# Kernel optimization log

Measured on AMD Instinct MI355X. Metric: run time of the kernel, lower is better.

## Reference

```python
import jax, jax.numpy as jnp
import numpy as np

N_A, N_B = 50000, 20000   # authors, teams
E0, E1, E2 = 600000, 300000, 300000  # coauthor(A->A), writes(A->B), influences(B->A)
D = 128                   # in_feats = out_feats


def setup_inputs() -> dict:
    key = jax.random.key(0)
    ks = jax.random.split(key, 12)
    h_A = jax.random.normal(ks[0], (N_A, D), jnp.float32)
    h_B = jax.random.normal(ks[1], (N_B, D), jnp.float32)
    W0 = jax.random.normal(ks[2], (D, D), jnp.float32) * 0.05
    W1 = jax.random.normal(ks[3], (D, D), jnp.float32) * 0.05
    W2 = jax.random.normal(ks[4], (D, D), jnp.float32) * 0.05
    b0 = jnp.zeros((D,), jnp.float32)
    b1 = jnp.zeros((D,), jnp.float32)
    b2 = jnp.zeros((D,), jnp.float32)
    src0 = jax.random.randint(ks[5], (E0,), 0, N_A)
    dst0 = jax.random.randint(ks[6], (E0,), 0, N_A)
    src1 = jax.random.randint(ks[7], (E1,), 0, N_A)
    dst1 = jax.random.randint(ks[8], (E1,), 0, N_B)
    src2 = jax.random.randint(ks[9], (E2,), 0, N_B)
    dst2 = jax.random.randint(ks[10], (E2,), 0, N_A)
    return dict(h_A=h_A, h_B=h_B, W0=W0, b0=b0, W1=W1, b1=b1, W2=W2, b2=b2,
                src0=src0, dst0=dst0, src1=src1, dst1=dst1, src2=src2, dst2=dst2)


def _graph_conv(x_src, W, b, src, dst, n_dst):
    """DGL GraphConv, norm='both': out = D_dst^{-1/2} A D_src^{-1/2} (X W) + b."""
    n_src = x_src.shape[0]
    ones = jnp.ones(src.shape[0], x_src.dtype)
    deg_out = jnp.clip(jax.ops.segment_sum(ones, src, num_segments=n_src), 1.0)
    deg_in = jnp.clip(jax.ops.segment_sum(ones, dst, num_segments=n_dst), 1.0)
    m = (x_src @ W) * (deg_out ** -0.5)[:, None]          # [n_src, D]
    agg = jax.ops.segment_sum(m[src], dst, num_segments=n_dst)  # [n_dst, D]
    return agg * (deg_in ** -0.5)[:, None] + b


def reference(h_A, h_B, W0, b0, W1, b1, W2, b2, src0, dst0, src1, dst1, src2, dst2):
    # HeteroGraphConv(aggregate='sum'): sum per-relation GraphConv outputs per dst ntype.
    out_A = (_graph_conv(h_A, W0, b0, src0, dst0, N_A)
             + _graph_conv(h_B, W2, b2, src2, dst2, N_A))
    out_B = _graph_conv(h_A, W1, b1, src1, dst1, N_B)
    # every ntype present in h receives an output, so no passthrough branch fires
    return out_A, out_B
```

## Files before the change

kernel.cpp:

```cpp
#include <hip/hip_runtime.h>

#define NA 50000
#define NB 20000
#define NE0 600000
#define NE1 300000
#define NE2 300000
#define DD 128
#define DEG_TOT (4 * NA + 2 * NB)
#define SUB 16384
#define PER 18750

#define P_TOT 5440000

typedef short bf16x8 __attribute__((ext_vector_type(8)));
typedef float f32x4 __attribute__((ext_vector_type(4)));

__device__ __forceinline__ unsigned short f2bf(float f) {
    union { float f; unsigned int u; } v; v.f = f;
    unsigned int r = v.u + 0x7fffu + ((v.u >> 16) & 1u);
    return (unsigned short)(r >> 16);
}
__device__ __forceinline__ float bf2f(unsigned int u16) {
    union { float f; unsigned int u; } v; v.u = u16 << 16;
    return v.f;
}

__global__ __launch_bounds__(512) void hist_kernel(
    const int* __restrict__ s0, const int* __restrict__ d0,
    const int* __restrict__ s1, const int* __restrict__ d1,
    const int* __restrict__ s2, const int* __restrict__ d2,
    int* __restrict__ P,
    int* __restrict__ rank0, int* __restrict__ rank1, int* __restrict__ rank2)
{
    __shared__ int h[SUB];
    const int cfg = blockIdx.z;
    const int En[6] = {NE0, NE0, NE1, NE1, NE2, NE2};
    const int Kn[6] = {NA, NA, NA, NB, NB, NA};
    const int Gn[6] = {32, 32, 16, 16, 16, 16};
    const int Po[6] = {0, 1600000, 3200000, 4000000, 4320000, 4640000};
    int E = En[cfg], K = Kn[cfg], G = Gn[cfg];
    int sub = blockIdx.x, g = blockIdx.y;
    int nsub = (K + SUB - 1) / SUB;
    if (sub >= nsub || g >= G) return;
    const int* keys = cfg == 0 ? s0 : cfg == 1 ? d0 : cfg == 2 ? s1
                    : cfg == 3 ? d1 : cfg == 4 ? s2 : d2;
    int* rk = cfg == 1 ? rank0 : cfg == 3 ? rank1 : cfg == 5 ? rank2 : (int*)0;
    int lo = sub * SUB;
    int hi = min(K, lo + SUB);
    int cnt = hi - lo;
    for (int i = threadIdx.x; i < cnt; i += 512) h[i] = 0;
    __syncthreads();
    int e1 = min(E, g * PER + PER);
    for (int e = g * PER + threadIdx.x; e < e1; e += 512) {
        int k = keys[e];
        if (k >= lo && k < hi) {
            int r = atomicAdd(&h[k - lo], 1);
            if (rk) rk[e] = r;
        }
    }
    __syncthreads();
    int* outp = P + Po[cfg] + g * K + lo;
    for (int i = threadIdx.x; i < cnt; i += 512) outp[i] = h[i];
}

__global__ __launch_bounds__(256) void reduce_kernel(
    const int* __restrict__ P, int* __restrict__ ideg, float* __restrict__ rdeg)
{
    int i = blockIdx.x * 256 + threadIdx.x;
    if (i >= DEG_TOT) return;
    int h, k;
    if      (i < NA)            { h = 0; k = i; }
    else if (i < 2 * NA)        { h = 1; k = i - NA; }
    else if (i < 3 * NA)        { h = 2; k = i - 2 * NA; }
    else if (i < 3 * NA + NB)   { h = 3; k = i - 3 * NA; }
    else if (i < 3 * NA + 2*NB) { h = 4; k = i - 3 * NA - NB; }
    else                        { h = 5; k = i - 3 * NA - 2 * NB; }
    const int Po[6] = {0, 1600000, 3200000, 4000000, 4320000, 4640000};
    const int Gn[6] = {32, 32, 16, 16, 16, 16};
    const int Kn[6] = {NA, NA, NA, NB, NB, NA};
    const int* p = P + Po[h] + k;
    int K = Kn[h], G = Gn[h], s = 0;
    for (int g = 0; g < G; ++g) s += p[g * K];
    ideg[i] = s;
    rdeg[i] = rsqrtf(fmaxf((float)s, 1.f));
}

__global__ __launch_bounds__(256) void scan_reduce(
    const int* __restrict__ ideg, int* __restrict__ spart)
{
    __shared__ int lds[256];
    int y = blockIdx.y;
    const int off[3] = {NA, 3 * NA, 3 * NA + 2 * NB};
    const int nn[3]  = {NA, NB, NA};
    int n = nn[y];
    int b = blockIdx.x, t = threadIdx.x;
    if (b * 1024 >= n) return;
    const int* deg = ideg + off[y];
    int base = b * 1024 + t * 4;
    int s = 0;
    #pragma unroll
    for (int k = 0; k < 4; ++k) { int i = base + k; if (i < n) s += deg[i]; }
    lds[t] = s; __syncthreads();
    for (int o = 128; o > 0; o >>= 1) {
        if (t < o) lds[t] += lds[t + o];
        __syncthreads();
    }
    if (t == 0) spart[y * 64 + b] = lds[0];
}

__global__ void spine_kernel(int* __restrict__ spart) {
    int w = threadIdx.x >> 6, lane = threadIdx.x & 63;
    const int nblk[3] = {49, 20, 49};
    int n = nblk[w];
    int* p = spart + w * 64;
    int orig = (lane < n) ? p[lane] : 0;
    int v = orig;
    #pragma unroll
    for (int o = 1; o < 64; o <<= 1) {
        int u = __shfl_up(v, o);
        if (lane >= o) v += u;
    }
    if (lane < n) p[lane] = v - orig;
}

__global__ __launch_bounds__(256) void scan_final(
    const int* __restrict__ ideg, const int* __restrict__ spart,
    int* __restrict__ rp)
{
    __shared__ int lds[256];
    int y = blockIdx.y;
    const int off[3] = {NA, 3 * NA, 3 * NA + 2 * NB};
    const int nn[3]  = {NA, NB, NA};
    const int ro[3]  = {0, NA, NA + NB};
    int n = nn[y];
    int b = blockIdx.x, t = threadIdx.x;
    if (b * 1024 >= n) return;
    const int* deg = ideg + off[y];
    int* rowptr = rp + ro[y];
    int base = b * 1024 + t * 4;
    int v[4]; int tsum = 0;
    #pragma unroll
    for (int k = 0; k < 4; ++k) {
        v[k] = (base + k < n) ? deg[base + k] : 0;
        tsum += v[k];
    }
    lds[t] = tsum; __syncthreads();
    for (int o = 1; o < 256; o <<= 1) {
        int x = (t >= o) ? lds[t - o] : 0;
        __syncthreads();
        lds[t] += x;
        __syncthreads();
    }
    int run = lds[t] - tsum + spart[y * 64 + b];
    #pragma unroll
    for (int k = 0; k < 4; ++k) {
        if (base + k < n) rowptr[base + k] = run;
        run += v[k];
    }
}

__global__ __launch_bounds__(256) void offsets_kernel(
    int* __restrict__ P, const int* __restrict__ rp)
{
    int i = blockIdx.x * 256 + threadIdx.x;
    if (i >= 2 * NA + NB) return;
    int base, G, K, d, run;
    if (i < NA)           { base = 1600000; G = 32; K = NA; d = i;           run = rp[d]; }
    else if (i < NA + NB) { base = 4000000; G = 16; K = NB; d = i - NA;      run = rp[NA + d]; }
    else                  { base = 4640000; G = 16; K = NA; d = i - NA - NB; run = rp[NA + NB + d]; }
    int* p = P + base + d;
    for (int g = 0; g < G; ++g) {
        int t = p[g * K];
        p[g * K] = run;
        run += t;
    }
}

__global__ __launch_bounds__(512) void place_parallel(
    const int* __restrict__ s0, const int* __restrict__ d0,
    const int* __restrict__ s1, const int* __restrict__ d1,
    const int* __restrict__ s2, const int* __restrict__ d2,
    const int* __restrict__ P,
    const int* __restrict__ rank0, const int* __restrict__ rank1,
    const int* __restrict__ rank2,
    int* __restrict__ csr0, int* __restrict__ csr1, int* __restrict__ csr2)
{
    int z = blockIdx.z;
    const int En[3] = {NE0, NE1, NE2};
    const int Kn[3] = {NA, NB, NA};
    const int Po[3] = {1600000, 4000000, 4640000};
    int E = En[z], K = Kn[z];
    const int* src = z == 0 ? s0 : z == 1 ? s1 : s2;
    const int* dst = z == 0 ? d0 : z == 1 ? d1 : d2;
    const int* rk  = z == 0 ? rank0 : z == 1 ? rank1 : rank2;
    int* csr = z == 0 ? csr0 : z == 1 ? csr1 : csr2;
    const int* off = P + Po[z];
    int e = blockIdx.x * 512 + threadIdx.x;
    if (e >= E) return;
    int d = dst[e];
    int g = e / PER;
    int pos = off[g * K + d] + rk[e];
    csr[pos] = src[e];
}

__global__ __launch_bounds__(256) void wt_kernel(
    const float* __restrict__ W0, const float* __restrict__ W1,
    const float* __restrict__ W2, unsigned short* __restrict__ Wt)
{
    int i = blockIdx.x * 256 + threadIdx.x;
    if (i >= 3 * DD * DD) return;
    int w = i >> 14, r = i & (DD * DD - 1);
    int c = r >> 7, k = r & (DD - 1);
    const float* W = (w == 0) ? W0 : ((w == 1) ? W1 : W2);
    Wt[i] = f2bf(W[k * DD + c]);
}

__global__ __launch_bounds__(256) void mfma_gemmA(
    const float* __restrict__ hA, const unsigned short* __restrict__ Wt,
    const float* __restrict__ rdeg,
    unsigned short* __restrict__ mA0, unsigned short* __restrict__ mA1)
{
    int wid  = threadIdx.x >> 6;
    int lane = threadIdx.x & 63;
    int quad = lane >> 4;
    int l16  = lane & 15;
    int base = blockIdx.x * 64 + wid * 16;
    if (base >= NA) return;

    int arow = base + l16;
    if (arow >= NA) arow = NA - 1;
    bf16x8 a[4];
    #pragma unroll
    for (int kk = 0; kk < 4; ++kk) {
        const float4* p = (const float4*)(hA + (size_t)arow * DD + kk * 32 + quad * 8);
        float4 u = p[0], w = p[1];
        bf16x8 t;
        t[0] = (short)f2bf(u.x); t[1] = (short)f2bf(u.y);
        t[2] = (short)f2bf(u.z); t[3] = (short)f2bf(u.w);
        t[4] = (short)f2bf(w.x); t[5] = (short)f2bf(w.y);
        t[6] = (short)f2bf(w.z); t[7] = (short)f2bf(w.w);
        a[kk] = t;
    }

    float rs0[4], rs1[4]; int orow0 = base + quad * 4;
    #pragma unroll
    for (int r = 0; r < 4; ++r) {
        int orow = orow0 + r; int c = orow < NA ? orow : 0;
        rs0[r] = rdeg[c]; rs1[r] = rdeg[2 * NA + c];
    }

    #pragma unroll
    for (int ct = 0; ct < 8; ++ct) {
        f32x4 acc0 = {0.f, 0.f, 0.f, 0.f};
        f32x4 acc1 = {0.f, 0.f, 0.f, 0.f};
        const unsigned short* wp = Wt + (size_t)(ct * 16 + l16) * DD + quad * 8;
        #pragma unroll
        for (int kk = 0; kk < 4; ++kk) {
            bf16x8 b0 = *(const bf16x8*)(wp + kk * 32);
            bf16x8 b1 = *(const bf16x8*)(wp + 16384 + kk * 32);
            acc0 = __builtin_amdgcn_mfma_f32_16x16x32_bf16(a[kk], b0, acc0, 0, 0, 0);
            acc1 = __builtin_amdgcn_mfma_f32_16x16x32_bf16(a[kk], b1, acc1, 0, 0, 0);
        }
        #pragma unroll
        for (int r = 0; r < 4; ++r) {
            int orow = orow0 + r;
            if (orow < NA) {
                mA0[(size_t)orow * DD + ct * 16 + l16] = f2bf(acc0[r] * rs0[r]);
                mA1[(size_t)orow * DD + ct * 16 + l16] = f2bf(acc1[r] * rs1[r]);
            }
        }
    }
}

__global__ __launch_bounds__(256) void mfma_gemmB(
    const float* __restrict__ hB, const unsigned short* __restrict__ Wt,
    const float* __restrict__ rdeg, unsigned short* __restrict__ mB2)
{
    int wid  = threadIdx.x >> 6;
    int lane = threadIdx.x & 63;
    int quad = lane >> 4;
    int l16  = lane & 15;
    int base = blockIdx.x * 64 + wid * 16;
    if (base >= NB) return;

    int arow = base + l16;
    if (arow >= NB) arow = NB - 1;
    bf16x8 a[4];
    #pragma unroll
    for (int kk = 0; kk < 4; ++kk) {
        const float4* p = (const float4*)(hB + (size_t)arow * DD + kk * 32 + quad * 8);
        float4 u = p[0], w = p[1];
        bf16x8 t;
        t[0] = (short)f2bf(u.x); t[1] = (short)f2bf(u.y);
        t[2] = (short)f2bf(u.z); t[3] = (short)f2bf(u.w);
        t[4] = (short)f2bf(w.x); t[5] = (short)f2bf(w.y);
        t[6] = (short)f2bf(w.z); t[7] = (short)f2bf(w.w);
        a[kk] = t;
    }

    float rs[4]; int orow0 = base + quad * 4;
    #pragma unroll
    for (int r = 0; r < 4; ++r) {
        int orow = orow0 + r;
        rs[r] = rdeg[3 * NA + NB + (orow < NB ? orow : 0)];
    }

    #pragma unroll
    for (int ct = 0; ct < 8; ++ct) {
        f32x4 acc = {0.f, 0.f, 0.f, 0.f};
        const unsigned short* wp = Wt + 32768 + (size_t)(ct * 16 + l16) * DD + quad * 8;
        #pragma unroll
        for (int kk = 0; kk < 4; ++kk) {
            bf16x8 b = *(const bf16x8*)(wp + kk * 32);
            acc = __builtin_amdgcn_mfma_f32_16x16x32_bf16(a[kk], b, acc, 0, 0, 0);
        }
        #pragma unroll
        for (int r = 0; r < 4; ++r) {
            int orow = orow0 + r;
            if (orow < NB)
                mB2[(size_t)orow * DD + ct * 16 + l16] = f2bf(acc[r] * rs[r]);
        }
    }
}

__device__ __forceinline__ void gather_rel(
    const unsigned short* __restrict__ M, const int* __restrict__ csr,
    int st, int n, int lane, float& o0, float& o1)
{
    for (int ch = 0; ch < n; ch += 64) {
        int m = min(64, n - ch);
        int idx = csr[st + ch + (lane < m ? lane : m - 1)];
        for (int j = 0; j < m; j += 4) {
            int sA = __shfl(idx, j);
            int sB = __shfl(idx, (j + 1 < m) ? j + 1 : j);
            int sC = __shfl(idx, (j + 2 < m) ? j + 2 : j);
            int sD = __shfl(idx, (j + 3 < m) ? j + 3 : j);
            float wB = (j + 1 < m) ? 1.f : 0.f;
            float wC = (j + 2 < m) ? 1.f : 0.f;
            float wD = (j + 3 < m) ? 1.f : 0.f;
            unsigned int uA = *(const unsigned int*)(M + (size_t)sA * DD + lane * 2);
            unsigned int uB = *(const unsigned int*)(M + (size_t)sB * DD + lane * 2);
            unsigned int uC = *(const unsigned int*)(M + (size_t)sC * DD + lane * 2);
            unsigned int uD = *(const unsigned int*)(M + (size_t)sD * DD + lane * 2);
            o0 += bf2f(uA & 0xffff);
            o1 += bf2f(uA >> 16);
            o0 = fmaf(wB, bf2f(uB & 0xffff), o0);
            o1 = fmaf(wB, bf2f(uB >> 16),    o1);
            o0 = fmaf(wC, bf2f(uC & 0xffff), o0);
            o1 = fmaf(wC, bf2f(uC >> 16),    o1);
            o0 = fmaf(wD, bf2f(uD & 0xffff), o0);
            o1 = fmaf(wD, bf2f(uD >> 16),    o1);
        }
    }
}

__global__ __launch_bounds__(256) void gather_A(
    const unsigned short* __restrict__ mA0, const unsigned short* __restrict__ mB2,
    const int* __restrict__ csr0, const int* __restrict__ rp0, const int* __restrict__ dg0,
    const int* __restrict__ csr2, const int* __restrict__ rp2, const int* __restrict__ dg2,
    const float* __restrict__ rdin0, const float* __restrict__ rdin2,
    const float* __restrict__ b0, const float* __restrict__ b2,
    float* __restrict__ out)
{
    int wid = threadIdx.x >> 6, lane = threadIdx.x & 63;
    int d = blockIdx.x * 4 + wid;
    if (d >= NA) return;

    float a0 = 0.f, a1 = 0.f, c0 = 0.f, c1 = 0.f;
    gather_rel(mA0, csr0, rp0[d], dg0[d], lane, a0, a1);
    gather_rel(mB2, csr2, rp2[d], dg2[d], lane, c0, c1);

    float r0 = rdin0[d], r2 = rdin2[d];
    int col = lane * 2;
    float2 o;
    o.x = a0 * r0 + c0 * r2 + b0[col]     + b2[col];
    o.y = a1 * r0 + c1 * r2 + b0[col + 1] + b2[col + 1];
    *(float2*)(out + (size_t)d * DD + col) = o;
}

__global__ __launch_bounds__(256) void gather_B(
    const unsigned short* __restrict__ mA1,
    const int* __restrict__ csr1, const int* __restrict__ rp1, const int* __restrict__ dg1,
    const float* __restrict__ rdin1, const float* __restrict__ b1,
    float* __restrict__ out)
{
    int wid = threadIdx.x >> 6, lane = threadIdx.x & 63;
    int d = blockIdx.x * 4 + wid;
    if (d >= NB) return;

    float a0 = 0.f, a1 = 0.f;
    gather_rel(mA1, csr1, rp1[d], dg1[d], lane, a0, a1);

    float r1 = rdin1[d];
    int col = lane * 2;
    float2 o;
    o.x = a0 * r1 + b1[col];
    o.y = a1 * r1 + b1[col + 1];
    *(float2*)(out + (size_t)d * DD + col) = o;
}

extern "C" void kernel_launch(void* const* d_in, const int* in_sizes, int n_in,
                              void* d_out, int out_size, void* d_ws, size_t ws_size,
                              hipStream_t stream) {
    const float* hA = (const float*)d_in[0];
    const float* hB = (const float*)d_in[1];
    const float* W0 = (const float*)d_in[2];
    const float* b0 = (const float*)d_in[3];
    const float* W1 = (const float*)d_in[4];
    const float* b1 = (const float*)d_in[5];
    const float* W2 = (const float*)d_in[6];
    const float* b2 = (const float*)d_in[7];
    const int* s0 = (const int*)d_in[8];
    const int* d0 = (const int*)d_in[9];
    const int* s1 = (const int*)d_in[10];
    const int* d1 = (const int*)d_in[11];
    const int* s2 = (const int*)d_in[12];
    const int* d2 = (const int*)d_in[13];
    float* out = (float*)d_out;
    char* ws = (char*)d_ws;

    unsigned short* mA0 = (unsigned short*)(ws + 0);
    unsigned short* mA1 = (unsigned short*)(ws + 12800000);
    unsigned short* mB2 = (unsigned short*)(ws + 25600000);
    int*   P            = (int*)  (ws + 0);
    unsigned short* Wt  = (unsigned short*)(ws + 30720000);
    float* rdeg         = (float*)(ws + 30818304);
    int*   ideg         = (int*)  (ws + 31778304);
    int*   rp           = (int*)  (ws + 32738304);
    int*   spart        = (int*)  (ws + 33218304);
    int*   rank0        = (int*)  (ws + 33219328);
    int*   rank1        = (int*)  (ws + 35619328);
    int*   rank2        = (int*)  (ws + 36819328);
    int*   csr0         = (int*)  (ws + 38019328);
    int*   csr1         = (int*)  (ws + 40419328);
    int*   csr2         = (int*)  (ws + 41619328);

    const int* din0 = ideg + NA;
    const int* din1 = ideg + 3 * NA;
    const int* din2 = ideg + 3 * NA + 2 * NB;
    const float* rdin0 = rdeg + NA;
    const float* rdin1 = rdeg + 3 * NA;
    const float* rdin2 = rdeg + 3 * NA + 2 * NB;

    hist_kernel<<<dim3(4, 32, 6), 512, 0, stream>>>(s0, d0, s1, d1, s2, d2,
                                                    P, rank0, rank1, rank2);
    reduce_kernel<<<(DEG_TOT + 255) / 256, 256, 0, stream>>>(P, ideg, rdeg);

    scan_reduce<<<dim3(49, 3), 256, 0, stream>>>(ideg, spart);
    spine_kernel<<<1, 192, 0, stream>>>(spart);
    scan_final<<<dim3(49, 3), 256, 0, stream>>>(ideg, spart, rp);

    offsets_kernel<<<(2 * NA + NB + 255) / 256, 256, 0, stream>>>(P, rp);
    place_parallel<<<dim3((NE0 + 511) / 512, 1, 3), 512, 0, stream>>>(
        s0, d0, s1, d1, s2, d2, P, rank0, rank1, rank2, csr0, csr1, csr2);

    wt_kernel<<<(3 * DD * DD + 255) / 256, 256, 0, stream>>>(W0, W1, W2, Wt);
    mfma_gemmA<<<(NA + 63) / 64, 256, 0, stream>>>(hA, Wt, rdeg, mA0, mA1);
    mfma_gemmB<<<(NB + 63) / 64, 256, 0, stream>>>(hB, Wt, rdeg, mB2);

    gather_A<<<(NA + 3) / 4, 256, 0, stream>>>(mA0, mB2,
        csr0, rp, din0, csr2, rp + NA + NB, din2, rdin0, rdin2, b0, b2, out);
    gather_B<<<(NB + 3) / 4, 256, 0, stream>>>(mA1,
        csr1, rp + NA, din1, rdin1, b1, out + (size_t)NA * DD);
}
```

Baseline: 286.6 us.

## Pack histogram counters as 16-bit, merge GEMM and gather launches

The histogram now packs two 16-bit counters per shared-memory word, so one block covers twice as many keys with 1024 threads. Partial counts are stored as 16-bit values, and offsets go to a separate int buffer. The two GEMM kernels are merged into one launch, as are the two gather kernels, which removes launch gaps and tail effects. The gather inner loop drops the predicated tail weights and uses simpler byte-offset addressing. The 16-bit counts assume no key appears more than 65535 times within one chunk, and the packed halves depend on the per-chunk key counts being even.

```diff
diff --git a/kernel.cpp b/kernel.cpp
--- a/kernel.cpp
+++ b/kernel.cpp
@@ -7,10 +7,9 @@
 #define NE2 300000
 #define DD 128
 #define DEG_TOT (4 * NA + 2 * NB)
-#define SUB 16384
+#define SUB 32768
 #define PER 18750
 
-#define P_TOT 5440000
 
 typedef short bf16x8 __attribute__((ext_vector_type(8)));
 typedef float f32x4 __attribute__((ext_vector_type(4)));
@@ -24,15 +23,23 @@
     union { float f; unsigned int u; } v; v.u = u16 << 16;
     return v.f;
 }
-
-__global__ __launch_bounds__(512) void hist_kernel(
+__device__ __forceinline__ float lo2f(unsigned int u) {
+    union { float f; unsigned int u; } v; v.u = u << 16;
+    return v.f;
+}
+__device__ __forceinline__ float hi2f(unsigned int u) {
+    union { float f; unsigned int u; } v; v.u = u & 0xffff0000u;
+    return v.f;
+}
+
+__global__ __launch_bounds__(1024) void hist_kernel(
     const int* __restrict__ s0, const int* __restrict__ d0,
     const int* __restrict__ s1, const int* __restrict__ d1,
     const int* __restrict__ s2, const int* __restrict__ d2,
-    int* __restrict__ P,
+    unsigned int* __restrict__ Pd,
     int* __restrict__ rank0, int* __restrict__ rank1, int* __restrict__ rank2)
 {
-    __shared__ int h[SUB];
+    __shared__ unsigned int h32[SUB / 2];
     const int cfg = blockIdx.z;
     const int En[6] = {NE0, NE0, NE1, NE1, NE2, NE2};
     const int Kn[6] = {NA, NA, NA, NB, NB, NA};
@@ -48,23 +55,26 @@
     int lo = sub * SUB;
     int hi = min(K, lo + SUB);
     int cnt = hi - lo;
-    for (int i = threadIdx.x; i < cnt; i += 512) h[i] = 0;
+    for (int i = threadIdx.x; i < SUB / 2; i += 1024) h32[i] = 0;
     __syncthreads();
     int e1 = min(E, g * PER + PER);
-    for (int e = g * PER + threadIdx.x; e < e1; e += 512) {
+    for (int e = g * PER + threadIdx.x; e < e1; e += 1024) {
         int k = keys[e];
         if (k >= lo && k < hi) {
-            int r = atomicAdd(&h[k - lo], 1);
-            if (rk) rk[e] = r;
+            int kk = k - lo;
+            unsigned sh = (kk & 1) << 4;
+            unsigned old = atomicAdd(&h32[kk >> 1], 1u << sh);
+            if (rk) rk[e] = (int)((old >> sh) & 0xffffu);
         }
     }
     __syncthreads();
-    int* outp = P + Po[cfg] + g * K + lo;
-    for (int i = threadIdx.x; i < cnt; i += 512) outp[i] = h[i];
+    unsigned int* outp = Pd + ((Po[cfg] + g * K + lo) >> 1);
+    for (int i = threadIdx.x; i < cnt / 2; i += 1024) outp[i] = h32[i];
 }
 
 __global__ __launch_bounds__(256) void reduce_kernel(
-    const int* __restrict__ P, int* __restrict__ ideg, float* __restrict__ rdeg)
+    const unsigned short* __restrict__ P16, int* __restrict__ ideg,
+    float* __restrict__ rdeg)
 {
     int i = blockIdx.x * 256 + threadIdx.x;
     if (i >= DEG_TOT) return;
@@ -78,7 +88,7 @@
     const int Po[6] = {0, 1600000, 3200000, 4000000, 4320000, 4640000};
     const int Gn[6] = {32, 32, 16, 16, 16, 16};
     const int Kn[6] = {NA, NA, NA, NB, NB, NA};
-    const int* p = P + Po[h] + k;
+    const unsigned short* p = P16 + Po[h] + k;
     int K = Kn[h], G = Gn[h], s = 0;
     for (int g = 0; g < G; ++g) s += p[g * K];
     ideg[i] = s;
@@ -160,18 +170,20 @@
 }
 
 __global__ __launch_bounds__(256) void offsets_kernel(
-    int* __restrict__ P, const int* __restrict__ rp)
+    const unsigned short* __restrict__ P16, const int* __restrict__ rp,
+    int* __restrict__ O)
 {
     int i = blockIdx.x * 256 + threadIdx.x;
     if (i >= 2 * NA + NB) return;
-    int base, G, K, d, run;
-    if (i < NA)           { base = 1600000; G = 32; K = NA; d = i;           run = rp[d]; }
-    else if (i < NA + NB) { base = 4000000; G = 16; K = NB; d = i - NA;      run = rp[NA + d]; }
-    else                  { base = 4640000; G = 16; K = NA; d = i - NA - NB; run = rp[NA + NB + d]; }
-    int* p = P + base + d;
+    int pbase, obase, G, K, d, run;
+    if (i < NA)           { pbase = 1600000; obase = 0;       G = 32; K = NA; d = i;           run = rp[d]; }
+    else if (i < NA + NB) { pbase = 4000000; obase = 1600000; G = 16; K = NB; d = i - NA;      run = rp[NA + d]; }
+    else                  { pbase = 4640000; obase = 1920000; G = 16; K = NA; d = i - NA - NB; run = rp[NA + NB + d]; }
+    const unsigned short* p = P16 + pbase + d;
+    int* o = O + obase + d;
     for (int g = 0; g < G; ++g) {
         int t = p[g * K];
-        p[g * K] = run;
+        o[g * K] = run;
         run += t;
     }
 }
@@ -180,7 +192,7 @@
     const int* __restrict__ s0, const int* __restrict__ d0,
     const int* __restrict__ s1, const int* __restrict__ d1,
     const int* __restrict__ s2, const int* __restrict__ d2,
-    const int* __restrict__ P,
+    const int* __restrict__ O,
     const int* __restrict__ rank0, const int* __restrict__ rank1,
     const int* __restrict__ rank2,
     int* __restrict__ csr0, int* __restrict__ csr1, int* __restrict__ csr2)
@@ -188,13 +200,13 @@
     int z = blockIdx.z;
     const int En[3] = {NE0, NE1, NE2};
     const int Kn[3] = {NA, NB, NA};
-    const int Po[3] = {1600000, 4000000, 4640000};
+    const int Oo[3] = {0, 1600000, 1920000};
     int E = En[z], K = Kn[z];
     const int* src = z == 0 ? s0 : z == 1 ? s1 : s2;
     const int* dst = z == 0 ? d0 : z == 1 ? d1 : d2;
     const int* rk  = z == 0 ? rank0 : z == 1 ? rank1 : rank2;
     int* csr = z == 0 ? csr0 : z == 1 ? csr1 : csr2;
-    const int* off = P + Po[z];
+    const int* off = O + Oo[z];
     int e = blockIdx.x * 512 + threadIdx.x;
     if (e >= E) return;
     int d = dst[e];
@@ -215,188 +227,170 @@
     Wt[i] = f2bf(W[k * DD + c]);
 }
 
-__global__ __launch_bounds__(256) void mfma_gemmA(
-    const float* __restrict__ hA, const unsigned short* __restrict__ Wt,
-    const float* __restrict__ rdeg,
-    unsigned short* __restrict__ mA0, unsigned short* __restrict__ mA1)
+__global__ __launch_bounds__(256) void gemm_all(
+    const float* __restrict__ hA, const float* __restrict__ hB,
+    const unsigned short* __restrict__ Wt, const float* __restrict__ rdeg,
+    unsigned short* __restrict__ mA0, unsigned short* __restrict__ mA1,
+    unsigned short* __restrict__ mB2)
 {
     int wid  = threadIdx.x >> 6;
     int lane = threadIdx.x & 63;
     int quad = lane >> 4;
     int l16  = lane & 15;
-    int base = blockIdx.x * 64 + wid * 16;
-    if (base >= NA) return;
-
-    int arow = base + l16;
-    if (arow >= NA) arow = NA - 1;
-    bf16x8 a[4];
-    #pragma unroll
-    for (int kk = 0; kk < 4; ++kk) {
-        const float4* p = (const float4*)(hA + (size_t)arow * DD + kk * 32 + quad * 8);
-        float4 u = p[0], w = p[1];
-        bf16x8 t;
-        t[0] = (short)f2bf(u.x); t[1] = (short)f2bf(u.y);
-        t[2] = (short)f2bf(u.z); t[3] = (short)f2bf(u.w);
-        t[4] = (short)f2bf(w.x); t[5] = (short)f2bf(w.y);
-        t[6] = (short)f2bf(w.z); t[7] = (short)f2bf(w.w);
-        a[kk] = t;
-    }
-
-    float rs0[4], rs1[4]; int orow0 = base + quad * 4;
-    #pragma unroll
-    for (int r = 0; r < 4; ++r) {
-        int orow = orow0 + r; int c = orow < NA ? orow : 0;
-        rs0[r] = rdeg[c]; rs1[r] = rdeg[2 * NA + c];
-    }
-
-    #pragma unroll
-    for (int ct = 0; ct < 8; ++ct) {
-        f32x4 acc0 = {0.f, 0.f, 0.f, 0.f};
-        f32x4 acc1 = {0.f, 0.f, 0.f, 0.f};
-        const unsigned short* wp = Wt + (size_t)(ct * 16 + l16) * DD + quad * 8;
+
+    if (blockIdx.x < 782) {
+        int base = blockIdx.x * 64 + wid * 16;
+        if (base >= NA) return;
+        int arow = base + l16;
+        if (arow >= NA) arow = NA - 1;
+        bf16x8 a[4];
         #pragma unroll
         for (int kk = 0; kk < 4; ++kk) {
-            bf16x8 b0 = *(const bf16x8*)(wp + kk * 32);
-            bf16x8 b1 = *(const bf16x8*)(wp + 16384 + kk * 32);
-            acc0 = __builtin_amdgcn_mfma_f32_16x16x32_bf16(a[kk], b0, acc0, 0, 0, 0);
-            acc1 = __builtin_amdgcn_mfma_f32_16x16x32_bf16(a[kk], b1, acc1, 0, 0, 0);
-        }
+            const float4* p = (const float4*)(hA + (size_t)arow * DD + kk * 32 + quad * 8);
+            float4 u = p[0], w = p[1];
+            bf16x8 t;
+            t[0] = (short)f2bf(u.x); t[1] = (short)f2bf(u.y);
+            t[2] = (short)f2bf(u.z); t[3] = (short)f2bf(u.w);
+            t[4] = (short)f2bf(w.x); t[5] = (short)f2bf(w.y);
+            t[6] = (short)f2bf(w.z); t[7] = (short)f2bf(w.w);
+            a[kk] = t;
+        }
+        float rs0[4], rs1[4]; int orow0 = base + quad * 4;
+        #pragma unroll
+        for (int r = 0; r < 4; ++r) {
+            int orow = orow0 + r; int c = orow < NA ? orow : 0;
+            rs0[r] = rdeg[c]; rs1[r] = rdeg[2 * NA + c];
+        }
+        #pragma unroll
+        for (int ct = 0; ct < 8; ++ct) {
+            f32x4 acc0 = {0.f, 0.f, 0.f, 0.f};
+            f32x4 acc1 = {0.f, 0.f, 0.f, 0.f};
+            const unsigned short* wp = Wt + (size_t)(ct * 16 + l16) * DD + quad * 8;
+            #pragma unroll
+            for (int kk = 0; kk < 4; ++kk) {
+                bf16x8 b0 = *(const bf16x8*)(wp + kk * 32);
+                bf16x8 b1 = *(const bf16x8*)(wp + 16384 + kk * 32);
+                acc0 = __builtin_amdgcn_mfma_f32_16x16x32_bf16(a[kk], b0, acc0, 0, 0, 0);
+                acc1 = __builtin_amdgcn_mfma_f32_16x16x32_bf16(a[kk], b1, acc1, 0, 0, 0);
+            }
+            #pragma unroll
+            for (int r = 0; r < 4; ++r) {
+                int orow = orow0 + r;
+                if (orow < NA) {
+                    mA0[(size_t)orow * DD + ct * 16 + l16] = f2bf(acc0[r] * rs0[r]);
+                    mA1[(size_t)orow * DD + ct * 16 + l16] = f2bf(acc1[r] * rs1[r]);
+                }
+            }
+        }
+    } else {
+        int base = (blockIdx.x - 782) * 64 + wid * 16;
+        if (base >= NB) return;
+        int arow = base + l16;
+        if (arow >= NB) arow = NB - 1;
+        bf16x8 a[4];
+        #pragma unroll
+        for (int kk = 0; kk < 4; ++kk) {
+            const float4* p = (const float4*)(hB + (size_t)arow * DD + kk * 32 + quad * 8);
+            float4 u = p[0], w = p[1];
+            bf16x8 t;
+            t[0] = (short)f2bf(u.x); t[1] = (short)f2bf(u.y);
+            t[2] = (short)f2bf(u.z); t[3] = (short)f2bf(u.w);
+            t[4] = (short)f2bf(w.x); t[5] = (short)f2bf(w.y);
+            t[6] = (short)f2bf(w.z); t[7] = (short)f2bf(w.w);
+            a[kk] = t;
+        }
+        float rs[4]; int orow0 = base + quad * 4;
         #pragma unroll
         for (int r = 0; r < 4; ++r) {
             int orow = orow0 + r;
-            if (orow < NA) {
-                mA0[(size_t)orow * DD + ct * 16 + l16] = f2bf(acc0[r] * rs0[r]);
-                mA1[(size_t)orow * DD + ct * 16 + l16] = f2bf(acc1[r] * rs1[r]);
+            rs[r] = rdeg[3 * NA + NB + (orow < NB ? orow : 0)];
+        }
+        #pragma unroll
+        for (int ct = 0; ct < 8; ++ct) {
+            f32x4 acc = {0.f, 0.f, 0.f, 0.f};
+            const unsigned short* wp = Wt + 32768 + (size_t)(ct * 16 + l16) * DD + quad * 8;
+            #pragma unroll
+            for (int kk = 0; kk < 4; ++kk) {
+                bf16x8 b = *(const bf16x8*)(wp + kk * 32);
+                acc = __builtin_amdgcn_mfma_f32_16x16x32_bf16(a[kk], b, acc, 0, 0, 0);
             }
-        }
-    }
-}
-
-__global__ __launch_bounds__(256) void mfma_gemmB(
-    const float* __restrict__ hB, const unsigned short* __restrict__ Wt,
-    const float* __restrict__ rdeg, unsigned short* __restrict__ mB2)
-{
-    int wid  = threadIdx.x >> 6;
-    int lane = threadIdx.x & 63;
-    int quad = lane >> 4;
-    int l16  = lane & 15;
-    int base = blockIdx.x * 64 + wid * 16;
-    if (base >= NB) return;
-
-    int arow = base + l16;
-    if (arow >= NB) arow = NB - 1;
-    bf16x8 a[4];
-    #pragma unroll
-    for (int kk = 0; kk < 4; ++kk) {
-        const float4* p = (const float4*)(hB + (size_t)arow * DD + kk * 32 + quad * 8);
-        float4 u = p[0], w = p[1];
-        bf16x8 t;
-        t[0] = (short)f2bf(u.x); t[1] = (short)f2bf(u.y);
-        t[2] = (short)f2bf(u.z); t[3] = (short)f2bf(u.w);
-        t[4] = (short)f2bf(w.x); t[5] = (short)f2bf(w.y);
-        t[6] = (short)f2bf(w.z); t[7] = (short)f2bf(w.w);
-        a[kk] = t;
-    }
-
-    float rs[4]; int orow0 = base + quad * 4;
-    #pragma unroll
-    for (int r = 0; r < 4; ++r) {
-        int orow = orow0 + r;
-        rs[r] = rdeg[3 * NA + NB + (orow < NB ? orow : 0)];
-    }
-
-    #pragma unroll
-    for (int ct = 0; ct < 8; ++ct) {
-        f32x4 acc = {0.f, 0.f, 0.f, 0.f};
-        const unsigned short* wp = Wt + 32768 + (size_t)(ct * 16 + l16) * DD + quad * 8;
-        #pragma unroll
-        for (int kk = 0; kk < 4; ++kk) {
-            bf16x8 b = *(const bf16x8*)(wp + kk * 32);
-            acc = __builtin_amdgcn_mfma_f32_16x16x32_bf16(a[kk], b, acc, 0, 0, 0);
-        }
-        #pragma unroll
-        for (int r = 0; r < 4; ++r) {
-            int orow = orow0 + r;
-            if (orow < NB)
-                mB2[(size_t)orow * DD + ct * 16 + l16] = f2bf(acc[r] * rs[r]);
+            #pragma unroll
+            for (int r = 0; r < 4; ++r) {
+                int orow = orow0 + r;
+                if (orow < NB)
+                    mB2[(size_t)orow * DD + ct * 16 + l16] = f2bf(acc[r] * rs[r]);
+            }
         }
     }
 }
 
 __device__ __forceinline__ void gather_rel(
-    const unsigned short* __restrict__ M, const int* __restrict__ csr,
-    int st, int n, int lane, float& o0, float& o1)
+    const char* __restrict__ Mb, const int* __restrict__ csr,
+    int st, int n, int lane, unsigned laneoff, float& o0, float& o1)
 {
     for (int ch = 0; ch < n; ch += 64) {
-        int m = min(64, n - ch);
+        int m = n - ch; if (m > 64) m = 64;
         int idx = csr[st + ch + (lane < m ? lane : m - 1)];
-        for (int j = 0; j < m; j += 4) {
+        int j = 0;
+        for (; j + 4 <= m; j += 4) {
             int sA = __shfl(idx, j);
-            int sB = __shfl(idx, (j + 1 < m) ? j + 1 : j);
-            int sC = __shfl(idx, (j + 2 < m) ? j + 2 : j);
-            int sD = __shfl(idx, (j + 3 < m) ? j + 3 : j);
-            float wB = (j + 1 < m) ? 1.f : 0.f;
-            float wC = (j + 2 < m) ? 1.f : 0.f;
-            float wD = (j + 3 < m) ? 1.f : 0.f;
-            unsigned int uA = *(const unsigned int*)(M + (size_t)sA * DD + lane * 2);
-            unsigned int uB = *(const unsigned int*)(M + (size_t)sB * DD + lane * 2);
-            unsigned int uC = *(const unsigned int*)(M + (size_t)sC * DD + lane * 2);
-            unsigned int uD = *(const unsigned int*)(M + (size_t)sD * DD + lane * 2);
-            o0 += bf2f(uA & 0xffff);
-            o1 += bf2f(uA >> 16);
-            o0 = fmaf(wB, bf2f(uB & 0xffff), o0);
-            o1 = fmaf(wB, bf2f(uB >> 16),    o1);
-            o0 = fmaf(wC, bf2f(uC & 0xffff), o0);
-            o1 = fmaf(wC, bf2f(uC >> 16),    o1);
-            o0 = fmaf(wD, bf2f(uD & 0xffff), o0);
-            o1 = fmaf(wD, bf2f(uD >> 16),    o1);
-        }
-    }
-}
-
-__global__ __launch_bounds__(256) void gather_A(
-    const unsigned short* __restrict__ mA0, const unsigned short* __restrict__ mB2,
-    const int* __restrict__ csr0, const int* __restrict__ rp0, const int* __restrict__ dg0,
-    const int* __restrict__ csr2, const int* __restrict__ rp2, const int* __restrict__ dg2,
-    const float* __restrict__ rdin0, const float* __restrict__ rdin2,
-    const float* __restrict__ b0, const float* __restrict__ b2,
+            int sB = __shfl(idx, j + 1);
+            int sC = __shfl(idx, j + 2);
+            int sD = __shfl(idx, j + 3);
+            unsigned uA = *(const unsigned*)(Mb + (((unsigned)sA << 8) + laneoff));
+            unsigned uB = *(const unsigned*)(Mb + (((unsigned)sB << 8) + laneoff));
+            unsigned uC = *(const unsigned*)(Mb + (((unsigned)sC << 8) + laneoff));
+            unsigned uD = *(const unsigned*)(Mb + (((unsigned)sD << 8) + laneoff));
+            o0 += lo2f(uA); o1 += hi2f(uA);
+            o0 += lo2f(uB); o1 += hi2f(uB);
+            o0 += lo2f(uC); o1 += hi2f(uC);
+            o0 += lo2f(uD); o1 += hi2f(uD);
+        }
+        for (; j < m; ++j) {
+            int s = __shfl(idx, j);
+            unsigned u = *(const unsigned*)(Mb + (((unsigned)s << 8) + laneoff));
+            o0 += lo2f(u); o1 += hi2f(u);
+        }
+    }
+}
+
+__global__ __launch_bounds__(256) void gather_all(
+    const unsigned short* __restrict__ mA0, const unsigned short* __restrict__ mA1,
+    const unsigned short* __restrict__ mB2,
+    const int* __restrict__ csr0, const int* __restrict__ csr1,
+    const int* __restrict__ csr2,
+    const int* __restrict__ rp, const int* __restrict__ ideg,
+    const float* __restrict__ rdeg,
+    const float* __restrict__ b0, const float* __restrict__ b1,
+    const float* __restrict__ b2,
     float* __restrict__ out)
 {
     int wid = threadIdx.x >> 6, lane = threadIdx.x & 63;
-    int d = blockIdx.x * 4 + wid;
-    if (d >= NA) return;
-
-    float a0 = 0.f, a1 = 0.f, c0 = 0.f, c1 = 0.f;
-    gather_rel(mA0, csr0, rp0[d], dg0[d], lane, a0, a1);
-    gather_rel(mB2, csr2, rp2[d], dg2[d], lane, c0, c1);
-
-    float r0 = rdin0[d], r2 = rdin2[d];
+    unsigned laneoff = (unsigned)lane * 4u;
     int col = lane * 2;
-    float2 o;
-    o.x = a0 * r0 + c0 * r2 + b0[col]     + b2[col];
-    o.y = a1 * r0 + c1 * r2 + b0[col + 1] + b2[col + 1];
-    *(float2*)(out + (size_t)d * DD + col) = o;
-}
-
-__global__ __launch_bounds__(256) void gather_B(
-    const unsigned short* __restrict__ mA1,
-    const int* __restrict__ csr1, const int* __restrict__ rp1, const int* __restrict__ dg1,
-    const float* __restrict__ rdin1, const float* __restrict__ b1,
-    float* __restrict__ out)
-{
-    int wid = threadIdx.x >> 6, lane = threadIdx.x & 63;
-    int d = blockIdx.x * 4 + wid;
-    if (d >= NB) return;
-
-    float a0 = 0.f, a1 = 0.f;
-    gather_rel(mA1, csr1, rp1[d], dg1[d], lane, a0, a1);
-
-    float r1 = rdin1[d];
-    int col = lane * 2;
-    float2 o;
-    o.x = a0 * r1 + b1[col];
-    o.y = a1 * r1 + b1[col + 1];
-    *(float2*)(out + (size_t)d * DD + col) = o;
+
+    if (blockIdx.x < 12500) {
+        int d = blockIdx.x * 4 + wid;
+        float a0 = 0.f, a1 = 0.f, c0 = 0.f, c1 = 0.f;
+        gather_rel((const char*)mA0, csr0, rp[d], ideg[NA + d], lane, laneoff, a0, a1);
+        gather_rel((const char*)mB2, csr2, rp[NA + NB + d], ideg[3 * NA + 2 * NB + d],
+                   lane, laneoff, c0, c1);
+        float r0 = rdeg[NA + d], r2 = rdeg[3 * NA + 2 * NB + d];
+        float2 o;
+        o.x = a0 * r0 + c0 * r2 + b0[col]     + b2[col];
+        o.y = a1 * r0 + c1 * r2 + b0[col + 1] + b2[col + 1];
+        *(float2*)(out + (size_t)d * DD + col) = o;
+    } else {
+        int d = (blockIdx.x - 12500) * 4 + wid;
+        float a0 = 0.f, a1 = 0.f;
+        gather_rel((const char*)mA1, csr1, rp[NA + d], ideg[3 * NA + d],
+                   lane, laneoff, a0, a1);
+        float r1 = rdeg[3 * NA + d];
+        float2 o;
+        o.x = a0 * r1 + b1[col];
+        o.y = a1 * r1 + b1[col + 1];
+        *(float2*)(out + (size_t)(NA + d) * DD + col) = o;
+    }
 }
 
 extern "C" void kernel_launch(void* const* d_in, const int* in_sizes, int n_in,
@@ -422,7 +416,9 @@
     unsigned short* mA0 = (unsigned short*)(ws + 0);
     unsigned short* mA1 = (unsigned short*)(ws + 12800000);
     unsigned short* mB2 = (unsigned short*)(ws + 25600000);
-    int*   P            = (int*)  (ws + 0);
+    unsigned short* P16 = (unsigned short*)(ws + 0);
+    unsigned int*   Pd  = (unsigned int*)(ws + 0);
+    int*   O            = (int*)  (ws + 10880000);
     unsigned short* Wt  = (unsigned short*)(ws + 30720000);
     float* rdeg         = (float*)(ws + 30818304);
     int*   ideg         = (int*)  (ws + 31778304);
@@ -435,31 +431,21 @@
     int*   csr1         = (int*)  (ws + 40419328);
     int*   csr2         = (int*)  (ws + 41619328);
 
-    const int* din0 = ideg + NA;
-    const int* din1 = ideg + 3 * NA;
-    const int* din2 = ideg + 3 * NA + 2 * NB;
-    const float* rdin0 = rdeg + NA;
-    const float* rdin1 = rdeg + 3 * NA;
-    const float* rdin2 = rdeg + 3 * NA + 2 * NB;
-
-    hist_kernel<<<dim3(4, 32, 6), 512, 0, stream>>>(s0, d0, s1, d1, s2, d2,
-                                                    P, rank0, rank1, rank2);
-    reduce_kernel<<<(DEG_TOT + 255) / 256, 256, 0, stream>>>(P, ideg, rdeg);
+    hist_kernel<<<dim3(2, 32, 6), 1024, 0, stream>>>(s0, d0, s1, d1, s2, d2,
+                                                     Pd, rank0, rank1, rank2);
+    reduce_kernel<<<(DEG_TOT + 255) / 256, 256, 0, stream>>>(P16, ideg, rdeg);
 
     scan_reduce<<<dim3(49, 3), 256, 0, stream>>>(ideg, spart);
     spine_kernel<<<1, 192, 0, stream>>>(spart);
     scan_final<<<dim3(49, 3), 256, 0, stream>>>(ideg, spart, rp);
 
-    offsets_kernel<<<(2 * NA + NB + 255) / 256, 256, 0, stream>>>(P, rp);
+    offsets_kernel<<<(2 * NA + NB + 255) / 256, 256, 0, stream>>>(P16, rp, O);
     place_parallel<<<dim3((NE0 + 511) / 512, 1, 3), 512, 0, stream>>>(
-        s0, d0, s1, d1, s2, d2, P, rank0, rank1, rank2, csr0, csr1, csr2);
+        s0, d0, s1, d1, s2, d2, O, rank0, rank1, rank2, csr0, csr1, csr2);
 
     wt_kernel<<<(3 * DD * DD + 255) / 256, 256, 0, stream>>>(W0, W1, W2, Wt);
-    mfma_gemmA<<<(NA + 63) / 64, 256, 0, stream>>>(hA, Wt, rdeg, mA0, mA1);
-    mfma_gemmB<<<(NB + 63) / 64, 256, 0, stream>>>(hB, Wt, rdeg, mB2);
-
-    gather_A<<<(NA + 3) / 4, 256, 0, stream>>>(mA0, mB2,
-        csr0, rp, din0, csr2, rp + NA + NB, din2, rdin0, rdin2, b0, b2, out);
-    gather_B<<<(NB + 3) / 4, 256, 0, stream>>>(mA1,
-        csr1, rp + NA, din1, rdin1, b1, out + (size_t)NA * DD);
-}
+    gemm_all<<<782 + 313, 256, 0, stream>>>(hA, hB, Wt, rdeg, mA0, mA1, mB2);
+
+    gather_all<<<12500 + 5000, 256, 0, stream>>>(mA0, mA1, mB2,
+        csr0, csr1, csr2, rp, ideg, rdeg, b0, b1, b2, out);
+}
```

Measured after the change: 264.7 us. 1.08x faster.
